# Kernel tuning notes

Measured on AMD Instinct MI355X. Metric: run time of the kernel, lower is better.

## Reference

```python
import jax, jax.numpy as jnp
import numpy as np

ALPHA = 0.2  # LeakyReLU negative slope
NEG_INF = -9e15


def gat_layer(h_in, adj_mask, W, a, concat):
    """Classic pyGAT dense GraphAttentionLayer (eval mode, dropout=identity).
    h_in: [B, N, Fin], adj_mask: [N, N] bool, W: [Fin, Fout], a: [2*Fout, 1].
    """
    h = jnp.einsum('bnf,fo->bno', h_in, W)          # [B, N, Fout]
    Fo = W.shape[1]
    f1 = h @ a[:Fo, 0]                               # [B, N] scores for source
    f2 = h @ a[Fo:, 0]                               # [B, N] scores for target
    e = jax.nn.leaky_relu(f1[:, :, None] + f2[:, None, :], negative_slope=ALPHA)
    e = jnp.where(adj_mask[None, :, :], e, NEG_INF)  # mask non-edges
    attn = jax.nn.softmax(e, axis=-1)                # normalize over neighbors
    out = jnp.einsum('bij,bjo->bio', attn, h)        # weighted aggregation
    return jax.nn.elu(out) if concat else out


def setup_inputs() -> dict:
    key = jax.random.key(0)
    ks = jax.random.split(key, 7)
    B, T, N = 2, 17, 1024
    nfeat, nhid, nclass, nheads = 64, 64, 64, 4
    x = jax.random.normal(ks[0], (B, T, N, nfeat), dtype=jnp.float32)
    adj = jax.random.randint(ks[1], (N, N), 0, 2, dtype=jnp.int32)
    W_heads = jax.random.normal(ks[2], (nheads, nfeat, nhid), dtype=jnp.float32) / np.sqrt(nfeat)
    a_heads = jax.random.normal(ks[3], (nheads, 2 * nhid, 1), dtype=jnp.float32) / np.sqrt(2 * nhid)
    W_out = jax.random.normal(ks[4], (nhid * nheads, nclass), dtype=jnp.float32) / np.sqrt(nhid * nheads)
    a_out = jax.random.normal(ks[5], (2 * nclass, 1), dtype=jnp.float32) / np.sqrt(2 * nclass)
    return {"x": x, "adj": adj, "W_heads": W_heads, "a_heads": a_heads,
            "W_out": W_out, "a_out": a_out, "pred_step": 1}


def reference(x, adj, W_heads, a_heads, W_out, a_out, pred_step):
    B, T, N, F = x.shape
    Tp = T - pred_step
    mask = adj > 0
    # All time steps are independent -> fold (B, Tp) into one batch axis.
    xt = x[:, :Tp].reshape(B * Tp, N, F)
    nheads = W_heads.shape[0]
    heads = [gat_layer(xt, mask, W_heads[h], a_heads[h], concat=True)
             for h in range(nheads)]
    hcat = jnp.concatenate(heads, axis=-1)           # [B*Tp, N, nhid*nheads]
    out = jax.nn.relu(gat_layer(hcat, mask, W_out, a_out, concat=False))
    return out.reshape(B, Tp, N, -1)
```

## Files before the change

kernel.cpp:

```cpp
#include <hip/hip_runtime.h>
#include <hip/hip_bf16.h>

typedef short bf16x8 __attribute__((ext_vector_type(8)));
typedef float f32x4 __attribute__((ext_vector_type(4)));
typedef _Float16 half8 __attribute__((ext_vector_type(8)));
typedef _Float16 half4 __attribute__((ext_vector_type(4)));
typedef __fp16 cvt2_t __attribute__((ext_vector_type(2)));

#define N_NODES 1024
#define FDIM 64
#define NG 32
#define LOG2E 1.44269504088896f

__global__ __launch_bounds__(256) void k_prep(const int* __restrict__ adj,
                                              const float* __restrict__ Wh,
                                              const float* __restrict__ Wo,
                                              unsigned char* __restrict__ Mbyte,
                                              _Float16* __restrict__ wt1,
                                              _Float16* __restrict__ wt2) {
    const int bb = blockIdx.x, t = threadIdx.x;
    if (bb < 128) {
        int w = bb * 256 + t;
        const int* p = adj + (size_t)w * 32;
        unsigned r[8];
#pragma unroll
        for (int q = 0; q < 8; q++) {
            int4 a = ((const int4*)p)[q];
            r[q] = (a.x > 0 ? 1u : 0u) | (a.y > 0 ? 1u << 8 : 0u) |
                   (a.z > 0 ? 1u << 16 : 0u) | (a.w > 0 ? 1u << 24 : 0u);
        }
        uint4* dst = (uint4*)(Mbyte + (size_t)w * 32);
        dst[0] = (uint4){r[0], r[1], r[2], r[3]};
        dst[1] = (uint4){r[4], r[5], r[6], r[7]};
    } else if (bb < 132) {
        const int row = (bb - 128) * 64 + (t >> 2);
        const int kq = t & 3;
        const float* src = Wh + (size_t)(row >> 6) * 4096 + (row & 63);
#pragma unroll
        for (int kk = 0; kk < 16; kk += 8) {
            const int k0 = kq * 16 + kk;
            union { half8 v; cvt2_t c[4]; } pk_;
#pragma unroll
            for (int j = 0; j < 8; j += 2)
                pk_.c[j >> 1] = __builtin_amdgcn_cvt_pkrtz(src[(k0 + j) * 64],
                                                           src[(k0 + j + 1) * 64]);
            *(half8*)(wt1 + (size_t)row * 64 + k0) = pk_.v;
        }
    } else {
        const int o = (bb - 132) * 16 + (t >> 4);
        const int k0 = (t & 15) * 16;
        const float* src = Wo + o;
#pragma unroll
        for (int kk = 0; kk < 16; kk += 8) {
            union { half8 v; cvt2_t c[4]; } pk_;
#pragma unroll
            for (int j = 0; j < 8; j += 2)
                pk_.c[j >> 1] = __builtin_amdgcn_cvt_pkrtz(src[(k0 + kk + j) * 64],
                                                           src[(k0 + kk + j + 1) * 64]);
            *(half8*)(wt2 + (size_t)o * 256 + k0 + kk) = pk_.v;
        }
    }
}

__global__ __launch_bounds__(512, 2) void k_proj1(const float* __restrict__ x,
                                                  const _Float16* __restrict__ wt1,
                                                  const float* __restrict__ ah,
                                                  _Float16* __restrict__ H1T,
                                                  float* __restrict__ Kv,
                                                  float* __restrict__ EB,
                                                  float* __restrict__ ED) {
    __shared__ _Float16 xs[128][64];
    const int t = threadIdx.x;
    const int nb = blockIdx.x, g = blockIdx.y;
    const int n0 = nb * 128;
    const int b = g >> 4, tstep = g & 15;

    {
        const int r = t >> 2, cq = t & 3;
        const float* xr = x + (((size_t)(b * 17 + tstep) * N_NODES + n0 + r) * FDIM) + cq * 16;
        float4 v0 = *(const float4*)(xr);
        float4 v1 = *(const float4*)(xr + 4);
        float4 v2 = *(const float4*)(xr + 8);
        float4 v3 = *(const float4*)(xr + 12);
        union { half8 v; cvt2_t c[4]; } u0, u1;
        u0.c[0] = __builtin_amdgcn_cvt_pkrtz(v0.x, v0.y);
        u0.c[1] = __builtin_amdgcn_cvt_pkrtz(v0.z, v0.w);
        u0.c[2] = __builtin_amdgcn_cvt_pkrtz(v1.x, v1.y);
        u0.c[3] = __builtin_amdgcn_cvt_pkrtz(v1.z, v1.w);
        u1.c[0] = __builtin_amdgcn_cvt_pkrtz(v2.x, v2.y);
        u1.c[1] = __builtin_amdgcn_cvt_pkrtz(v2.z, v2.w);
        u1.c[2] = __builtin_amdgcn_cvt_pkrtz(v3.x, v3.y);
        u1.c[3] = __builtin_amdgcn_cvt_pkrtz(v3.z, v3.w);
        *(half8*)&xs[r][((2 * cq) ^ (r & 7)) * 8] = u0.v;
        *(half8*)&xs[r][((2 * cq + 1) ^ (r & 7)) * 8] = u1.v;
    }
    __syncthreads();

    const int wv = t >> 6, ln = t & 63, li = ln & 15, grp = ln >> 4;
    const int arow = wv * 16 + li;

    f32x4 acc[16];
#pragma unroll
    for (int q = 0; q < 16; q++) acc[q] = (f32x4){0.f, 0.f, 0.f, 0.f};

#pragma unroll
    for (int s = 0; s < 2; s++) {
        half8 af = *(const half8*)&xs[arow][((s * 4 + grp) ^ (arow & 7)) * 8];
#pragma unroll
        for (int tile = 0; tile < 16; tile++) {
            half8 bf = *(const half8*)(wt1 + (size_t)(tile * 16 + li) * 64 + s * 32 + grp * 8);
            acc[tile] = __builtin_amdgcn_mfma_f32_16x16x32_f16(af, bf, acc[tile], 0, 0, 0);
        }
    }

    const int nbase = n0 + wv * 16 + grp * 4;
#pragma unroll
    for (int h = 0; h < 4; h++) {
        float p1[4] = {0.f, 0.f, 0.f, 0.f}, p2[4] = {0.f, 0.f, 0.f, 0.f};
#pragma unroll
        for (int ot = 0; ot < 4; ot++) {
            float a1v = ah[h * 128 + ot * 16 + li];
            float a2v = ah[h * 128 + 64 + ot * 16 + li];
            f32x4 A = acc[h * 4 + ot];
#pragma unroll
            for (int r = 0; r < 4; r++) {
                p1[r] = fmaf(A[r], a1v, p1[r]);
                p2[r] = fmaf(A[r], a2v, p2[r]);
            }
        }
#pragma unroll
        for (int m = 1; m < 16; m <<= 1)
#pragma unroll
            for (int r = 0; r < 4; r++) {
                p1[r] += __shfl_xor(p1[r], m);
                p2[r] += __shfl_xor(p2[r], m);
            }
        if (li == 0) {
            const size_t gh = (size_t)h * NG + g;
#pragma unroll
            for (int r = 0; r < 4; r++) {
                float phi1 = p1[r] * LOG2E, phi2 = p2[r] * LOG2E;
                Kv[gh * N_NODES + nbase + r] = __builtin_amdgcn_exp2f(-0.8f * phi1);
                EB[gh * N_NODES + nbase + r] = __builtin_amdgcn_exp2f(phi2);
                ED[gh * N_NODES + nbase + r] = __builtin_amdgcn_exp2f(0.2f * phi2);
            }
        }
    }
#pragma unroll
    for (int tile = 0; tile < 16; tile++) {
        const int h = tile >> 2, ot = tile & 3;
        union { half4 v; cvt2_t c[2]; } st;
        st.c[0] = __builtin_amdgcn_cvt_pkrtz(acc[tile][0], acc[tile][1]);
        st.c[1] = __builtin_amdgcn_cvt_pkrtz(acc[tile][2], acc[tile][3]);
        _Float16* dst = H1T + (((size_t)h * NG + g) * FDIM + ot * 16 + li) * N_NODES + nbase;
        *(half4*)dst = st.v;
    }
}

template<int CONCAT>
__global__ __launch_bounds__(512, 4) void k_attn(
    const _Float16* __restrict__ HT,
    const float* __restrict__ Kv,
    const float* __restrict__ EB,
    const float* __restrict__ ED,
    const unsigned char* __restrict__ Mb,
    _Float16* __restrict__ HC,
    float* __restrict__ out)
{
    __shared__ _Float16 vt[64][256];
    __shared__ float ebs[N_NODES];
    __shared__ float eds[N_NODES];
    const int t = threadIdx.x;
    const int g = blockIdx.x, h = blockIdx.y, nb = blockIdx.z;
    const int i0 = nb * 128;
    const size_t gidx = CONCAT ? ((size_t)h * NG + g) : (size_t)g;

    ((float2*)ebs)[t] = ((const float2*)(EB + gidx * N_NODES))[t];
    ((float2*)eds)[t] = ((const float2*)(ED + gidx * N_NODES))[t];

    const int wv = t >> 6, ln = t & 63;
    const int li = ln & 15, grp = ln >> 4, jb = grp * 8;
    const int lx = li & 7;
    const int il = wv * 16 + li;
    const float kv_ = Kv[gidx * N_NODES + i0 + il];

    const _Float16* Hg = HT + gidx * (size_t)(FDIM * N_NODES);
    const int srow = wv * 8 + (ln >> 3);
    const int swu = (ln & 7) ^ (srow & 7);
    const _Float16* srcb = Hg + (size_t)srow * N_NODES + (ln & 7) * 8;
    const unsigned char* Mrow = Mb + (size_t)(i0 + il) * N_NODES + jb;

    f32x4 acc[4], acc5;
#pragma unroll
    for (int q = 0; q < 4; q++) acc[q] = (f32x4){0.f, 0.f, 0.f, 0.f};
    acc5 = (f32x4){0.f, 0.f, 0.f, 0.f};

    union { half8 v; unsigned short s[8]; } onesu;
#pragma unroll
    for (int q = 0; q < 8; q++) onesu.s[q] = 0x3C00;
    const half8 ones = onesu.v;

    half8 stg[4];
    uint2 mbuf[2][8];
#pragma unroll
    for (int k2 = 0; k2 < 4; k2++) stg[k2] = *(const half8*)(srcb + k2 * 64);
#pragma unroll
    for (int q = 0; q < 8; q++) mbuf[0][q] = *(const uint2*)(Mrow + q * 32);

#pragma unroll
    for (int jt = 0; jt < 4; jt++) {
        __syncthreads();
#pragma unroll
        for (int k2 = 0; k2 < 4; k2++)
            *(half8*)&vt[srow][(k2 * 8 + swu) * 8] = stg[k2];
        if (jt < 3) {
#pragma unroll
            for (int k2 = 0; k2 < 4; k2++)
                stg[k2] = *(const half8*)(srcb + (jt + 1) * 256 + k2 * 64);
#pragma unroll
            for (int q = 0; q < 8; q++)
                mbuf[(jt + 1) & 1][q] = *(const uint2*)(Mrow + (jt + 1) * 256 + q * 32);
        }
        __syncthreads();

#pragma unroll
        for (int jc = 0; jc < 8; jc++) {
            const uint2 w = mbuf[jt & 1][jc];
            const float* ebp = &ebs[jt * 256 + jc * 32 + jb];
            const float* edp = &eds[jt * 256 + jc * 32 + jb];
            float4 ea0 = *(const float4*)ebp;
            float4 ea1 = *(const float4*)(ebp + 4);
            float4 ec0 = *(const float4*)edp;
            float4 ec1 = *(const float4*)(edp + 4);

            float b0 = (float)(unsigned char)(w.x);
            float b1 = (float)(unsigned char)(w.x >> 8);
            float b2 = (float)(unsigned char)(w.x >> 16);
            float b3 = (float)(w.x >> 24);
            float b4 = (float)(unsigned char)(w.y);
            float b5 = (float)(unsigned char)(w.y >> 8);
            float b6 = (float)(unsigned char)(w.y >> 16);
            float b7 = (float)(w.y >> 24);

            float q0 = fmaxf(ea0.x, kv_ * ec0.x) * b0;
            float q1 = fmaxf(ea0.y, kv_ * ec0.y) * b1;
            float q2 = fmaxf(ea0.z, kv_ * ec0.z) * b2;
            float q3 = fmaxf(ea0.w, kv_ * ec0.w) * b3;
            float q4 = fmaxf(ea1.x, kv_ * ec1.x) * b4;
            float q5 = fmaxf(ea1.y, kv_ * ec1.y) * b5;
            float q6 = fmaxf(ea1.z, kv_ * ec1.z) * b6;
            float q7 = fmaxf(ea1.w, kv_ * ec1.w) * b7;

            union { half8 v; cvt2_t c[4]; } afr;
            afr.c[0] = __builtin_amdgcn_cvt_pkrtz(q0, q1);
            afr.c[1] = __builtin_amdgcn_cvt_pkrtz(q2, q3);
            afr.c[2] = __builtin_amdgcn_cvt_pkrtz(q4, q5);
            afr.c[3] = __builtin_amdgcn_cvt_pkrtz(q6, q7);

            const int ub = (jc >> 1) * 8 + (((jc & 1) * 4 + grp) ^ lx);
#pragma unroll
            for (int q = 0; q < 4; q++) {
                half8 bfr = *(const half8*)&vt[q * 16 + li][ub * 8];
                acc[q] = __builtin_amdgcn_mfma_f32_16x16x32_f16(afr.v, bfr, acc[q], 0, 0, 0);
            }
            acc5 = __builtin_amdgcn_mfma_f32_16x16x32_f16(afr.v, ones, acc5, 0, 0, 0);
        }
    }

    float rin[4];
#pragma unroll
    for (int r2 = 0; r2 < 4; r2++) rin[r2] = 1.0f / acc5[r2];

    if (CONCAT) {
        _Float16* HCg = HC + (size_t)g * N_NODES * 256 + h * 64;
#pragma unroll
        for (int q = 0; q < 4; q++)
#pragma unroll
            for (int r2 = 0; r2 < 4; r2++) {
                int irow = wv * 16 + grp * 4 + r2;
                float v = acc[q][r2] * rin[r2];
                v = v > 0.f ? v : expm1f(v);
                HCg[(size_t)(i0 + irow) * 256 + q * 16 + li] = (_Float16)v;
            }
    } else {
        float* og = out + (size_t)g * N_NODES * FDIM;
#pragma unroll
        for (int q = 0; q < 4; q++)
#pragma unroll
            for (int r2 = 0; r2 < 4; r2++) {
                int irow = wv * 16 + grp * 4 + r2;
                float v = acc[q][r2] * rin[r2];
                og[(size_t)(i0 + irow) * FDIM + q * 16 + li] = v > 0.f ? v : 0.f;
            }
    }
}

__global__ __launch_bounds__(512, 2) void k_proj2(const _Float16* __restrict__ HC,
                                                  const _Float16* __restrict__ wt2,
                                                  const float* __restrict__ ao,
                                                  _Float16* __restrict__ H2T,
                                                  float* __restrict__ Kv2,
                                                  float* __restrict__ EB2,
                                                  float* __restrict__ ED2) {
    __shared__ _Float16 xs[128][256];
    const int t = threadIdx.x;
    const int nb = blockIdx.x, g = blockIdx.y;
    const int n0 = nb * 128;

    {
        const int r = t >> 2, cq = t & 3;
        const _Float16* src = HC + ((size_t)g * N_NODES + n0 + r) * 256 + cq * 64;
#pragma unroll
        for (int uu = 0; uu < 8; uu++) {
            int u = cq * 8 + uu;
            half8 v = *(const half8*)(src + uu * 8);
            int us = (u & 24) | ((u ^ r) & 7);
            *(half8*)&xs[r][us * 8] = v;
        }
    }
    __syncthreads();

    const int wv = t >> 6, ln = t & 63, li = ln & 15, grp = ln >> 4;
    const int arow = wv * 16 + li;

    f32x4 acc[4];
#pragma unroll
    for (int q = 0; q < 4; q++) acc[q] = (f32x4){0.f, 0.f, 0.f, 0.f};

#pragma unroll
    for (int s = 0; s < 8; s++) {
        int u = s * 4 + grp;
        int us = (u & 24) | ((u ^ arow) & 7);
        half8 af = *(const half8*)&xs[arow][us * 8];
#pragma unroll
        for (int tile = 0; tile < 4; tile++) {
            half8 bf = *(const half8*)(wt2 + (size_t)(tile * 16 + li) * 256 + s * 32 + grp * 8);
            acc[tile] = __builtin_amdgcn_mfma_f32_16x16x32_f16(af, bf, acc[tile], 0, 0, 0);
        }
    }

    const int nbase = n0 + wv * 16 + grp * 4;
    {
        float p1[4] = {0.f, 0.f, 0.f, 0.f}, p2[4] = {0.f, 0.f, 0.f, 0.f};
#pragma unroll
        for (int ot = 0; ot < 4; ot++) {
            float a1v = ao[ot * 16 + li];
            float a2v = ao[64 + ot * 16 + li];
            f32x4 A = acc[ot];
#pragma unroll
            for (int r = 0; r < 4; r++) {
                p1[r] = fmaf(A[r], a1v, p1[r]);
                p2[r] = fmaf(A[r], a2v, p2[r]);
            }
        }
#pragma unroll
        for (int m = 1; m < 16; m <<= 1)
#pragma unroll
            for (int r = 0; r < 4; r++) {
                p1[r] += __shfl_xor(p1[r], m);
                p2[r] += __shfl_xor(p2[r], m);
            }
        if (li == 0) {
#pragma unroll
            for (int r = 0; r < 4; r++) {
                float phi1 = p1[r] * LOG2E, phi2 = p2[r] * LOG2E;
                Kv2[(size_t)g * N_NODES + nbase + r] = __builtin_amdgcn_exp2f(-0.8f * phi1);
                EB2[(size_t)g * N_NODES + nbase + r] = __builtin_amdgcn_exp2f(phi2);
                ED2[(size_t)g * N_NODES + nbase + r] = __builtin_amdgcn_exp2f(0.2f * phi2);
            }
        }
    }
#pragma unroll
    for (int tile = 0; tile < 4; tile++) {
        union { half4 v; cvt2_t c[2]; } st;
        st.c[0] = __builtin_amdgcn_cvt_pkrtz(acc[tile][0], acc[tile][1]);
        st.c[1] = __builtin_amdgcn_cvt_pkrtz(acc[tile][2], acc[tile][3]);
        _Float16* dst = H2T + ((size_t)g * FDIM + tile * 16 + li) * N_NODES + nbase;
        *(half4*)dst = st.v;
    }
}

extern "C" void kernel_launch(void* const* d_in, const int* in_sizes, int n_in,
                              void* d_out, int out_size, void* d_ws, size_t ws_size,
                              hipStream_t stream) {
    const float* x  = (const float*)d_in[0];
    const int* adj  = (const int*)d_in[1];
    const float* Wh = (const float*)d_in[2];
    const float* ah = (const float*)d_in[3];
    const float* Wo = (const float*)d_in[4];
    const float* ao = (const float*)d_in[5];

    char* ws = (char*)d_ws;
    unsigned char* Mbyte = (unsigned char*)(ws);
    _Float16* wt1 = (_Float16*)(ws + 1048576);
    _Float16* wt2 = (_Float16*)(ws + 1081344);
    float* Kv1 = (float*)(ws + 1114112);
    float* EB1 = (float*)(ws + 1638400);
    float* ED1 = (float*)(ws + 2162688);
    float* Kv2 = (float*)(ws + 2686976);
    float* EB2 = (float*)(ws + 2818048);
    float* ED2 = (float*)(ws + 2949120);
    _Float16* H1T = (_Float16*)(ws + 3080192);
    _Float16* HC  = (_Float16*)(ws + 3080192 + 16777216);
    _Float16* H2T = (_Float16*)(ws + 3080192 + 33554432);
    float* out = (float*)d_out;

    k_prep   <<<dim3(136),       dim3(256), 0, stream>>>(adj, Wh, Wo, Mbyte, wt1, wt2);
    k_proj1  <<<dim3(8, 32),     dim3(512), 0, stream>>>(x, wt1, ah, H1T, Kv1, EB1, ED1);
    k_attn<1><<<dim3(32, 4, 8),  dim3(512), 0, stream>>>(H1T, Kv1, EB1, ED1, Mbyte, HC, nullptr);
    k_proj2  <<<dim3(8, 32),     dim3(512), 0, stream>>>(HC, wt2, ao, H2T, Kv2, EB2, ED2);
    k_attn<0><<<dim3(32, 1, 8),  dim3(512), 0, stream>>>(H2T, Kv2, EB2, ED2, Mbyte, nullptr, out);
}
```

Measured before the change: 114.2 us.

## Process two row tiles per wave in attention and derive EB from ED

The attention kernel now covers 256 query rows per block, with each wave computing two 16-row tiles. Both tiles reuse the same shared-memory V fragments, which halves the grid along the row axis and cuts repeated staging of H. The EB array is removed: its value is recomputed as ED^5 in registers, which drops a global store, a global load and a shared array. The trade-offs are extra multiplies, higher register pressure (launch bounds lowered from 4 to 2 blocks), and a mask-prefetch buffer reduced to a shallow rolling window.

```diff
diff --git a/kernel.cpp b/kernel.cpp
--- a/kernel.cpp
+++ b/kernel.cpp
@@ -67,7 +67,6 @@
                                                   const float* __restrict__ ah,
                                                   _Float16* __restrict__ H1T,
                                                   float* __restrict__ Kv,
-                                                  float* __restrict__ EB,
                                                   float* __restrict__ ED) {
     __shared__ _Float16 xs[128][64];
     const int t = threadIdx.x;
@@ -141,7 +140,6 @@
             for (int r = 0; r < 4; r++) {
                 float phi1 = p1[r] * LOG2E, phi2 = p2[r] * LOG2E;
                 Kv[gh * N_NODES + nbase + r] = __builtin_amdgcn_exp2f(-0.8f * phi1);
-                EB[gh * N_NODES + nbase + r] = __builtin_amdgcn_exp2f(phi2);
                 ED[gh * N_NODES + nbase + r] = __builtin_amdgcn_exp2f(0.2f * phi2);
             }
         }
@@ -158,42 +156,45 @@
 }
 
 template<int CONCAT>
-__global__ __launch_bounds__(512, 4) void k_attn(
+__global__ __launch_bounds__(512, 2) void k_attn(
     const _Float16* __restrict__ HT,
     const float* __restrict__ Kv,
-    const float* __restrict__ EB,
     const float* __restrict__ ED,
     const unsigned char* __restrict__ Mb,
     _Float16* __restrict__ HC,
     float* __restrict__ out)
 {
     __shared__ _Float16 vt[64][256];
-    __shared__ float ebs[N_NODES];
     __shared__ float eds[N_NODES];
     const int t = threadIdx.x;
     const int g = blockIdx.x, h = blockIdx.y, nb = blockIdx.z;
-    const int i0 = nb * 128;
+    const int i0 = nb * 256;
     const size_t gidx = CONCAT ? ((size_t)h * NG + g) : (size_t)g;
 
-    ((float2*)ebs)[t] = ((const float2*)(EB + gidx * N_NODES))[t];
     ((float2*)eds)[t] = ((const float2*)(ED + gidx * N_NODES))[t];
 
     const int wv = t >> 6, ln = t & 63;
     const int li = ln & 15, grp = ln >> 4, jb = grp * 8;
     const int lx = li & 7;
-    const int il = wv * 16 + li;
-    const float kv_ = Kv[gidx * N_NODES + i0 + il];
+    const int rowa = i0 + wv * 32 + li;
+    const float kva = Kv[gidx * N_NODES + rowa];
+    const float kvb = Kv[gidx * N_NODES + rowa + 16];
 
     const _Float16* Hg = HT + gidx * (size_t)(FDIM * N_NODES);
     const int srow = wv * 8 + (ln >> 3);
     const int swu = (ln & 7) ^ (srow & 7);
     const _Float16* srcb = Hg + (size_t)srow * N_NODES + (ln & 7) * 8;
-    const unsigned char* Mrow = Mb + (size_t)(i0 + il) * N_NODES + jb;
-
-    f32x4 acc[4], acc5;
-#pragma unroll
-    for (int q = 0; q < 4; q++) acc[q] = (f32x4){0.f, 0.f, 0.f, 0.f};
-    acc5 = (f32x4){0.f, 0.f, 0.f, 0.f};
+    const unsigned char* Mra = Mb + (size_t)rowa * N_NODES + jb;
+    const unsigned char* Mrb = Mra + 16 * N_NODES;
+
+    f32x4 acca[4], accb[4], acc5a, acc5b;
+#pragma unroll
+    for (int q = 0; q < 4; q++) {
+        acca[q] = (f32x4){0.f, 0.f, 0.f, 0.f};
+        accb[q] = (f32x4){0.f, 0.f, 0.f, 0.f};
+    }
+    acc5a = (f32x4){0.f, 0.f, 0.f, 0.f};
+    acc5b = (f32x4){0.f, 0.f, 0.f, 0.f};
 
     union { half8 v; unsigned short s[8]; } onesu;
 #pragma unroll
@@ -201,11 +202,10 @@
     const half8 ones = onesu.v;
 
     half8 stg[4];
-    uint2 mbuf[2][8];
 #pragma unroll
     for (int k2 = 0; k2 < 4; k2++) stg[k2] = *(const half8*)(srcb + k2 * 64);
-#pragma unroll
-    for (int q = 0; q < 8; q++) mbuf[0][q] = *(const uint2*)(Mrow + q * 32);
+    uint2 ma0 = *(const uint2*)Mra, ma1 = *(const uint2*)(Mra + 32);
+    uint2 mb0 = *(const uint2*)Mrb, mb1 = *(const uint2*)(Mrb + 32);
 
 #pragma unroll
     for (int jt = 0; jt < 4; jt++) {
@@ -217,59 +217,76 @@
 #pragma unroll
             for (int k2 = 0; k2 < 4; k2++)
                 stg[k2] = *(const half8*)(srcb + (jt + 1) * 256 + k2 * 64);
-#pragma unroll
-            for (int q = 0; q < 8; q++)
-                mbuf[(jt + 1) & 1][q] = *(const uint2*)(Mrow + (jt + 1) * 256 + q * 32);
         }
         __syncthreads();
 
 #pragma unroll
         for (int jc = 0; jc < 8; jc++) {
-            const uint2 w = mbuf[jt & 1][jc];
-            const float* ebp = &ebs[jt * 256 + jc * 32 + jb];
+            const uint2 wa = ma0, wb = mb0;
+            ma0 = ma1; mb0 = mb1;
+            if (!(jt == 3 && jc >= 6)) {
+                ma1 = *(const uint2*)(Mra + 64);
+                mb1 = *(const uint2*)(Mrb + 64);
+            }
+            Mra += 32; Mrb += 32;
+
             const float* edp = &eds[jt * 256 + jc * 32 + jb];
-            float4 ea0 = *(const float4*)ebp;
-            float4 ea1 = *(const float4*)(ebp + 4);
             float4 ec0 = *(const float4*)edp;
             float4 ec1 = *(const float4*)(edp + 4);
-
-            float b0 = (float)(unsigned char)(w.x);
-            float b1 = (float)(unsigned char)(w.x >> 8);
-            float b2 = (float)(unsigned char)(w.x >> 16);
-            float b3 = (float)(w.x >> 24);
-            float b4 = (float)(unsigned char)(w.y);
-            float b5 = (float)(unsigned char)(w.y >> 8);
-            float b6 = (float)(unsigned char)(w.y >> 16);
-            float b7 = (float)(w.y >> 24);
-
-            float q0 = fmaxf(ea0.x, kv_ * ec0.x) * b0;
-            float q1 = fmaxf(ea0.y, kv_ * ec0.y) * b1;
-            float q2 = fmaxf(ea0.z, kv_ * ec0.z) * b2;
-            float q3 = fmaxf(ea0.w, kv_ * ec0.w) * b3;
-            float q4 = fmaxf(ea1.x, kv_ * ec1.x) * b4;
-            float q5 = fmaxf(ea1.y, kv_ * ec1.y) * b5;
-            float q6 = fmaxf(ea1.z, kv_ * ec1.z) * b6;
-            float q7 = fmaxf(ea1.w, kv_ * ec1.w) * b7;
-
-            union { half8 v; cvt2_t c[4]; } afr;
-            afr.c[0] = __builtin_amdgcn_cvt_pkrtz(q0, q1);
-            afr.c[1] = __builtin_amdgcn_cvt_pkrtz(q2, q3);
-            afr.c[2] = __builtin_amdgcn_cvt_pkrtz(q4, q5);
-            afr.c[3] = __builtin_amdgcn_cvt_pkrtz(q6, q7);
+            float ecv[8] = {ec0.x, ec0.y, ec0.z, ec0.w, ec1.x, ec1.y, ec1.z, ec1.w};
+            float e5[8];
+#pragma unroll
+            for (int e = 0; e < 8; e++) {
+                float t2 = ecv[e] * ecv[e];
+                e5[e] = t2 * t2 * ecv[e];
+            }
+            float ba[8], bb[8];
+            ba[0] = (float)(unsigned char)(wa.x);
+            ba[1] = (float)(unsigned char)(wa.x >> 8);
+            ba[2] = (float)(unsigned char)(wa.x >> 16);
+            ba[3] = (float)(wa.x >> 24);
+            ba[4] = (float)(unsigned char)(wa.y);
+            ba[5] = (float)(unsigned char)(wa.y >> 8);
+            ba[6] = (float)(unsigned char)(wa.y >> 16);
+            ba[7] = (float)(wa.y >> 24);
+            bb[0] = (float)(unsigned char)(wb.x);
+            bb[1] = (float)(unsigned char)(wb.x >> 8);
+            bb[2] = (float)(unsigned char)(wb.x >> 16);
+            bb[3] = (float)(wb.x >> 24);
+            bb[4] = (float)(unsigned char)(wb.y);
+            bb[5] = (float)(unsigned char)(wb.y >> 8);
+            bb[6] = (float)(unsigned char)(wb.y >> 16);
+            bb[7] = (float)(wb.y >> 24);
+
+            union { half8 v; cvt2_t c[4]; } afa, afb;
+#pragma unroll
+            for (int d = 0; d < 4; d++) {
+                float qa0 = fmaxf(e5[2 * d],     kva * ecv[2 * d])     * ba[2 * d];
+                float qa1 = fmaxf(e5[2 * d + 1], kva * ecv[2 * d + 1]) * ba[2 * d + 1];
+                afa.c[d] = __builtin_amdgcn_cvt_pkrtz(qa0, qa1);
+                float qb0 = fmaxf(e5[2 * d],     kvb * ecv[2 * d])     * bb[2 * d];
+                float qb1 = fmaxf(e5[2 * d + 1], kvb * ecv[2 * d + 1]) * bb[2 * d + 1];
+                afb.c[d] = __builtin_amdgcn_cvt_pkrtz(qb0, qb1);
+            }
 
             const int ub = (jc >> 1) * 8 + (((jc & 1) * 4 + grp) ^ lx);
 #pragma unroll
             for (int q = 0; q < 4; q++) {
                 half8 bfr = *(const half8*)&vt[q * 16 + li][ub * 8];
-                acc[q] = __builtin_amdgcn_mfma_f32_16x16x32_f16(afr.v, bfr, acc[q], 0, 0, 0);
-            }
-            acc5 = __builtin_amdgcn_mfma_f32_16x16x32_f16(afr.v, ones, acc5, 0, 0, 0);
-        }
-    }
-
-    float rin[4];
-#pragma unroll
-    for (int r2 = 0; r2 < 4; r2++) rin[r2] = 1.0f / acc5[r2];
+                acca[q] = __builtin_amdgcn_mfma_f32_16x16x32_f16(afa.v, bfr, acca[q], 0, 0, 0);
+                accb[q] = __builtin_amdgcn_mfma_f32_16x16x32_f16(afb.v, bfr, accb[q], 0, 0, 0);
+            }
+            acc5a = __builtin_amdgcn_mfma_f32_16x16x32_f16(afa.v, ones, acc5a, 0, 0, 0);
+            acc5b = __builtin_amdgcn_mfma_f32_16x16x32_f16(afb.v, ones, acc5b, 0, 0, 0);
+        }
+    }
+
+    float rina[4], rinb[4];
+#pragma unroll
+    for (int r2 = 0; r2 < 4; r2++) {
+        rina[r2] = 1.0f / acc5a[r2];
+        rinb[r2] = 1.0f / acc5b[r2];
+    }
 
     if (CONCAT) {
         _Float16* HCg = HC + (size_t)g * N_NODES * 256 + h * 64;
@@ -277,10 +294,13 @@
         for (int q = 0; q < 4; q++)
 #pragma unroll
             for (int r2 = 0; r2 < 4; r2++) {
-                int irow = wv * 16 + grp * 4 + r2;
-                float v = acc[q][r2] * rin[r2];
-                v = v > 0.f ? v : expm1f(v);
-                HCg[(size_t)(i0 + irow) * 256 + q * 16 + li] = (_Float16)v;
+                int ira = i0 + wv * 32 + grp * 4 + r2;
+                float va = acca[q][r2] * rina[r2];
+                va = va > 0.f ? va : expm1f(va);
+                HCg[(size_t)ira * 256 + q * 16 + li] = (_Float16)va;
+                float vb = accb[q][r2] * rinb[r2];
+                vb = vb > 0.f ? vb : expm1f(vb);
+                HCg[(size_t)(ira + 16) * 256 + q * 16 + li] = (_Float16)vb;
             }
     } else {
         float* og = out + (size_t)g * N_NODES * FDIM;
@@ -288,9 +308,11 @@
         for (int q = 0; q < 4; q++)
 #pragma unroll
             for (int r2 = 0; r2 < 4; r2++) {
-                int irow = wv * 16 + grp * 4 + r2;
-                float v = acc[q][r2] * rin[r2];
-                og[(size_t)(i0 + irow) * FDIM + q * 16 + li] = v > 0.f ? v : 0.f;
+                int ira = i0 + wv * 32 + grp * 4 + r2;
+                float va = acca[q][r2] * rina[r2];
+                og[(size_t)ira * FDIM + q * 16 + li] = va > 0.f ? va : 0.f;
+                float vb = accb[q][r2] * rinb[r2];
+                og[(size_t)(ira + 16) * FDIM + q * 16 + li] = vb > 0.f ? vb : 0.f;
             }
     }
 }
@@ -300,7 +322,6 @@
                                                   const float* __restrict__ ao,
                                                   _Float16* __restrict__ H2T,
                                                   float* __restrict__ Kv2,
-                                                  float* __restrict__ EB2,
                                                   float* __restrict__ ED2) {
     __shared__ _Float16 xs[128][256];
     const int t = threadIdx.x;
@@ -365,7 +386,6 @@
             for (int r = 0; r < 4; r++) {
                 float phi1 = p1[r] * LOG2E, phi2 = p2[r] * LOG2E;
                 Kv2[(size_t)g * N_NODES + nbase + r] = __builtin_amdgcn_exp2f(-0.8f * phi1);
-                EB2[(size_t)g * N_NODES + nbase + r] = __builtin_amdgcn_exp2f(phi2);
                 ED2[(size_t)g * N_NODES + nbase + r] = __builtin_amdgcn_exp2f(0.2f * phi2);
             }
         }
@@ -395,19 +415,17 @@
     _Float16* wt1 = (_Float16*)(ws + 1048576);
     _Float16* wt2 = (_Float16*)(ws + 1081344);
     float* Kv1 = (float*)(ws + 1114112);
-    float* EB1 = (float*)(ws + 1638400);
-    float* ED1 = (float*)(ws + 2162688);
-    float* Kv2 = (float*)(ws + 2686976);
-    float* EB2 = (float*)(ws + 2818048);
-    float* ED2 = (float*)(ws + 2949120);
-    _Float16* H1T = (_Float16*)(ws + 3080192);
-    _Float16* HC  = (_Float16*)(ws + 3080192 + 16777216);
-    _Float16* H2T = (_Float16*)(ws + 3080192 + 33554432);
+    float* ED1 = (float*)(ws + 1638400);
+    float* Kv2 = (float*)(ws + 2162688);
+    float* ED2 = (float*)(ws + 2293760);
+    _Float16* H1T = (_Float16*)(ws + 2424832);
+    _Float16* HC  = (_Float16*)(ws + 2424832 + 16777216);
+    _Float16* H2T = (_Float16*)(ws + 2424832 + 33554432);
     float* out = (float*)d_out;
 
     k_prep   <<<dim3(136),       dim3(256), 0, stream>>>(adj, Wh, Wo, Mbyte, wt1, wt2);
-    k_proj1  <<<dim3(8, 32),     dim3(512), 0, stream>>>(x, wt1, ah, H1T, Kv1, EB1, ED1);
-    k_attn<1><<<dim3(32, 4, 8),  dim3(512), 0, stream>>>(H1T, Kv1, EB1, ED1, Mbyte, HC, nullptr);
-    k_proj2  <<<dim3(8, 32),     dim3(512), 0, stream>>>(HC, wt2, ao, H2T, Kv2, EB2, ED2);
-    k_attn<0><<<dim3(32, 1, 8),  dim3(512), 0, stream>>>(H2T, Kv2, EB2, ED2, Mbyte, nullptr, out);
+    k_proj1  <<<dim3(8, 32),     dim3(512), 0, stream>>>(x, wt1, ah, H1T, Kv1, ED1);
+    k_attn<1><<<dim3(32, 4, 4),  dim3(512), 0, stream>>>(H1T, Kv1, ED1, Mbyte, HC, nullptr);
+    k_proj2  <<<dim3(8, 32),     dim3(512), 0, stream>>>(HC, wt2, ao, H2T, Kv2, ED2);
+    k_attn<0><<<dim3(32, 1, 4),  dim3(512), 0, stream>>>(H2T, Kv2, ED2, Mbyte, nullptr, out);
 }
```

After: 101.0 us. 1.13x faster.
